# Optimization experiments

Measured on AMD Instinct MI355X. Metric: run time of the kernel, lower is better.

## Reference

```python
import jax, jax.numpy as jnp
import numpy as np

NUM_CAPSULE = 16
DIM_CAPSULE = 32
ROUTINGS = 4
EPS = 1e-07


def squash(x, axis=-1):
    # NOTE: faithful to the source: x / sqrt(sum(x^2) + eps) (unit-norm style),
    # NOT the standard Hinton squash.
    s2 = jnp.sum(x * x, axis=axis, keepdims=True)
    return x / jnp.sqrt(s2 + EPS)


def setup_inputs() -> dict:
    key = jax.random.key(0)
    k1, k2 = jax.random.split(key)
    B, N_in, D_in = 128, 1024, 256
    x = jax.random.normal(k1, (B, N_in, D_in), dtype=jnp.float32)
    # xavier_normal over (1, D_in, NUM_CAPSULE*DIM_CAPSULE)
    fan_in, fan_out = D_in, NUM_CAPSULE * DIM_CAPSULE
    std = np.sqrt(2.0 / (fan_in + fan_out))
    W = jax.random.normal(k2, (1, D_in, NUM_CAPSULE * DIM_CAPSULE), dtype=jnp.float32) * std
    return {"x": x, "W": W}


def reference(x, W):
    B, N_in, _ = x.shape
    # u_hat: [B, N_in, num_cap*dim_cap] -> [B, num_cap, N_in, dim_cap]
    u_hat = jnp.matmul(x, W[0])
    u_hat = u_hat.reshape(B, N_in, NUM_CAPSULE, DIM_CAPSULE).transpose(0, 2, 1, 3)

    b = jnp.zeros((B, NUM_CAPSULE, N_in), dtype=u_hat.dtype)
    outputs = None
    for i in range(ROUTINGS):
        # torch permutes to softmax over the num_capsule axis; equivalent to axis=1 here
        c = jax.nn.softmax(b, axis=1)                      # [B, num_cap, N_in]
        outputs = squash(jnp.einsum('bij,bijk->bik', c, u_hat))  # [B, num_cap, dim_cap]
        if i < ROUTINGS - 1:
            b = jnp.einsum('bik,bijk->bij', outputs, u_hat)
    return outputs
```

## Files before the change

### kernel.cpp

```cpp
#include <hip/hip_runtime.h>
#include <hip/hip_bf16.h>

typedef unsigned int u32;
typedef float f32x4 __attribute__((ext_vector_type(4)));
typedef __bf16 bf16x8 __attribute__((ext_vector_type(8)));

#define BATCH 128
#define NIN   1024
#define DIN   256
#define NC    16
#define DC    32
#define NCOL  512

__device__ __forceinline__ float bflo(u32 v){ return __uint_as_float(v << 16); }
__device__ __forceinline__ float bfhi(u32 v){ return __uint_as_float(v & 0xffff0000u); }
__device__ __forceinline__ u32 bfround(u32 ua){ return (ua + 0x7fffu + ((ua >> 16) & 1u)) >> 16; }
__device__ __forceinline__ u32 pack2(float a, float b){
    return (bfround(__float_as_uint(a)) & 0xffffu) | (bfround(__float_as_uint(b)) << 16);
}
__device__ __forceinline__ bf16x8 ldfrag(const u32* p){
    return __builtin_bit_cast(bf16x8, *(const uint4*)p);
}

__global__ __launch_bounds__(256) void k_wconv(const float* __restrict__ W, uint4* __restrict__ Wt2){
    int id = blockIdx.x * 256 + threadIdx.x;
    int l = id & 63, ks = (id >> 6) & 7, ntile = id >> 9;
    int n = ntile * 16 + (l & 15);
    int w0 = ks * 16 + (l >> 4) * 4;
    u32 r[4];
    #pragma unroll
    for (int e = 0; e < 4; e++){
        int w = w0 + e;
        r[e] = pack2(W[(size_t)(2 * w) * NCOL + n], W[(size_t)(2 * w + 1) * NCOL + n]);
    }
    Wt2[id] = make_uint4(r[0], r[1], r[2], r[3]);
}

__global__ __launch_bounds__(512) void k_gemm(const float* __restrict__ x, const uint4* __restrict__ Wt2,
                                              u32* __restrict__ uhat, float* __restrict__ y0){
    __shared__ __align__(16) u32 xl[64 * 128];
    const int t = threadIdx.x, jb = blockIdx.x, b = blockIdx.y;
    const int lane = t & 63, wv = t >> 6;
    const int l15 = lane & 15, q = lane >> 4;

    {
        const float4* xg = (const float4*)(x + ((size_t)b * NIN + jb * 64) * DIN);
        #pragma unroll
        for (int m = 0; m < 4; m++){
            int p = t + 512 * m;
            float4 a = xg[2 * p], c = xg[2 * p + 1];
            int j = p >> 5, wq = 4 * (p & 31);
            uint4 v;
            v.x = pack2(a.x, a.y); v.y = pack2(a.z, a.w);
            v.z = pack2(c.x, c.y); v.w = pack2(c.z, c.w);
            *(uint4*)&xl[j * 128 + ((wq + 4 * j) & 127)] = v;
        }
    }
    __syncthreads();

    f32x4 acc[4][4];
    #pragma unroll
    for (int mt = 0; mt < 4; mt++)
        #pragma unroll
        for (int nt = 0; nt < 4; nt++) acc[mt][nt] = (f32x4){0.f, 0.f, 0.f, 0.f};
    #pragma unroll
    for (int ks = 0; ks < 8; ks++){
        bf16x8 af[4], bfr[4];
        #pragma unroll
        for (int mt = 0; mt < 4; mt++){
            int jr = mt * 16 + l15;
            af[mt] = ldfrag(&xl[jr * 128 + ((ks * 16 + q * 4 + 4 * jr) & 127)]);
        }
        #pragma unroll
        for (int nt = 0; nt < 4; nt++)
            bfr[nt] = __builtin_bit_cast(bf16x8, Wt2[(size_t)(((wv * 4 + nt) * 8 + ks) * 64) + lane]);
        #pragma unroll
        for (int mt = 0; mt < 4; mt++)
            #pragma unroll
            for (int nt = 0; nt < 4; nt++)
                acc[mt][nt] = __builtin_amdgcn_mfma_f32_16x16x32_bf16(af[mt], bfr[nt], acc[mt][nt], 0, 0, 0);
    }

    #pragma unroll
    for (int nt = 0; nt < 4; nt++){
        float v = 0.f;
        #pragma unroll
        for (int mt = 0; mt < 4; mt++)
            #pragma unroll
            for (int r = 0; r < 4; r++) v += acc[mt][nt][r];
        v += __shfl_xor(v, 16);
        v += __shfl_xor(v, 32);
        if (lane < 16) atomicAdd(&y0[b * NCOL + wv * 64 + nt * 16 + lane], v);
    }

    u32* ub = uhat + (((size_t)b * NC + jb) * NCOL) * 32;
    #pragma unroll
    for (int nt = 0; nt < 4; nt++){
        int n = wv * 64 + nt * 16 + l15;
        #pragma unroll
        for (int mt = 0; mt < 4; mt++){
            uint2 v;
            v.x = pack2(acc[mt][nt][0], acc[mt][nt][1]);
            v.y = pack2(acc[mt][nt][2], acc[mt][nt][3]);
            *(uint2*)&ub[n * 32 + mt * 8 + q * 2] = v;
        }
    }
}

__device__ __forceinline__ int rot8(int n){ return (n + (n >> 3)) & 7; }

__global__ __launch_bounds__(256) void k_route_u(const u32* __restrict__ uhat, const float* __restrict__ o,
                                                 float* __restrict__ y){
    __shared__ __align__(16) u32 ul[NCOL * 32];
    __shared__ float ol[NCOL];
    __shared__ float bbc[NC * 68];
    const int jc = blockIdx.x, b = blockIdx.y, t = threadIdx.x;

    ol[t] = o[b * NCOL + t];
    ol[t + 256] = o[b * NCOL + t + 256];
    {
        const uint4* ug = (const uint4*)(uhat + ((size_t)(b * NC + jc)) * NCOL * 32);
        #pragma unroll
        for (int m = 0; m < 16; m++){
            int id = t + 256 * m;
            int n = id >> 3, jq = id & 7;
            ((uint4*)ul)[n * 8 + ((jq + rot8(n)) & 7)] = ug[id];
        }
    }
    __syncthreads();

    {
        int i = t >> 4, jq2 = t & 15;
        float o_[32];
        #pragma unroll
        for (int e = 0; e < 8; e++) *(float4*)&o_[4 * e] = *(const float4*)&ol[i * DC + 4 * e];
        float a0 = 0.f, a1 = 0.f, a2 = 0.f, a3 = 0.f;
        #pragma unroll
        for (int k = 0; k < 32; k++){
            int n = i * DC + k;
            uint2 v = *(const uint2*)&ul[n * 32 + ((2 * jq2 + 4 * rot8(n)) & 31)];
            float ok = o_[k];
            a0 += ok * bflo(v.x); a1 += ok * bfhi(v.x);
            a2 += ok * bflo(v.y); a3 += ok * bfhi(v.y);
        }
        *(float4*)&bbc[i * 68 + 4 * jq2] = make_float4(a0, a1, a2, a3);
    }
    __syncthreads();

    if (t < 64){
        float m = -1e30f;
        #pragma unroll
        for (int i = 0; i < NC; i++) m = fmaxf(m, bbc[i * 68 + t]);
        float s = 0.f;
        #pragma unroll
        for (int i = 0; i < NC; i++){ float e = __expf(bbc[i * 68 + t] - m); bbc[i * 68 + t] = e; s += e; }
        float inv = 1.f / s;
        #pragma unroll
        for (int i = 0; i < NC; i++) bbc[i * 68 + t] *= inv;
    }
    __syncthreads();

    #pragma unroll
    for (int h = 0; h < 2; h++){
        int n = t + 256 * h;
        int i = n >> 5;
        float s = 0.f;
        #pragma unroll
        for (int w4 = 0; w4 < 8; w4++){
            uint4 v = *(const uint4*)&ul[n * 32 + ((4 * w4 + 4 * rot8(n)) & 31)];
            float4 c0 = *(const float4*)&bbc[i * 68 + 8 * w4];
            float4 c1 = *(const float4*)&bbc[i * 68 + 8 * w4 + 4];
            s += c0.x * bflo(v.x) + c0.y * bfhi(v.x) + c0.z * bflo(v.y) + c0.w * bfhi(v.y)
               + c1.x * bflo(v.z) + c1.y * bfhi(v.z) + c1.z * bflo(v.w) + c1.w * bfhi(v.w);
        }
        atomicAdd(&y[b * NCOL + n], s);
    }
}

__global__ __launch_bounds__(512) void k_squash(const float* __restrict__ y, float* __restrict__ o,
                                                float* __restrict__ out, int final){
    int b = blockIdx.x, t = threadIdx.x;
    float v = y[b * NCOL + t];
    float s = v * v;
    s += __shfl_xor(s, 1); s += __shfl_xor(s, 2); s += __shfl_xor(s, 4);
    s += __shfl_xor(s, 8); s += __shfl_xor(s, 16);
    float r = v / sqrtf(s + 1e-7f);
    if (final) out[b * NCOL + t] = r;
    else       o[b * NCOL + t] = r;
}

extern "C" void kernel_launch(void* const* d_in, const int* in_sizes, int n_in,
                              void* d_out, int out_size, void* d_ws, size_t ws_size,
                              hipStream_t stream){
    const float* x = (const float*)d_in[0];
    const float* W = (const float*)d_in[1];
    float* out = (float*)d_out;
    float* f = (float*)d_ws;
    float* y    = f;
    float* o    = f + 65536;
    uint4* Wt2  = (uint4*)(f + 131072);
    u32*   uhat = (u32*)(f + 196608);

    hipMemsetAsync(y, 0, NCOL * BATCH * sizeof(float), stream);
    k_wconv<<<64, 256, 0, stream>>>(W, Wt2);
    k_gemm<<<dim3(16, BATCH), 512, 0, stream>>>(x, Wt2, uhat, y);
    k_squash<<<BATCH, 512, 0, stream>>>(y, o, out, 0);
    for (int it = 1; it < 4; it++){
        hipMemsetAsync(y, 0, NCOL * BATCH * sizeof(float), stream);
        k_route_u<<<dim3(16, BATCH), 256, 0, stream>>>(uhat, o, y);
        k_squash<<<BATCH, 512, 0, stream>>>(y, o, out, it == 3 ? 1 : 0);
    }
}
```

Baseline: 323.3 us.

## Reassociate routing through W to avoid materializing u_hat

The materialized u_hat tensor is dropped. Routing is re-expressed algebraically: the agreement logits become x·(W·o), and the weighted sum becomes (c^T x)·W, so each iteration works on x (bf16, transposed copy) and small per-batch vectors. A pre-kernel converts x to bf16 and also transposes it. It computes column sums for the first uniform-coupling iteration and converts W. The main kernel runs both contractions with MFMA and writes partial sums that a tail kernel reduces, multiplies by W, squashes, and projects back to v = W·o. This removes the large u_hat write and its repeated reads, at the cost of extra passes over x per iteration and new rounding points.

```diff
diff --git a/kernel.cpp b/kernel.cpp
--- a/kernel.cpp
+++ b/kernel.cpp
@@ -1,7 +1,7 @@
 #include <hip/hip_runtime.h>
-#include <hip/hip_bf16.h>
 
 typedef unsigned int u32;
+typedef unsigned short u16;
 typedef float f32x4 __attribute__((ext_vector_type(4)));
 typedef __bf16 bf16x8 __attribute__((ext_vector_type(8)));
 
@@ -18,175 +18,179 @@
 __device__ __forceinline__ u32 pack2(float a, float b){
     return (bfround(__float_as_uint(a)) & 0xffffu) | (bfround(__float_as_uint(b)) << 16);
 }
-__device__ __forceinline__ bf16x8 ldfrag(const u32* p){
-    return __builtin_bit_cast(bf16x8, *(const uint4*)p);
-}
-
-__global__ __launch_bounds__(256) void k_wconv(const float* __restrict__ W, uint4* __restrict__ Wt2){
-    int id = blockIdx.x * 256 + threadIdx.x;
-    int l = id & 63, ks = (id >> 6) & 7, ntile = id >> 9;
-    int n = ntile * 16 + (l & 15);
-    int w0 = ks * 16 + (l >> 4) * 4;
-    u32 r[4];
-    #pragma unroll
-    for (int e = 0; e < 4; e++){
-        int w = w0 + e;
-        r[e] = pack2(W[(size_t)(2 * w) * NCOL + n], W[(size_t)(2 * w + 1) * NCOL + n]);
-    }
-    Wt2[id] = make_uint4(r[0], r[1], r[2], r[3]);
-}
-
-__global__ __launch_bounds__(512) void k_gemm(const float* __restrict__ x, const uint4* __restrict__ Wt2,
-                                              u32* __restrict__ uhat, float* __restrict__ y0){
-    __shared__ __align__(16) u32 xl[64 * 128];
-    const int t = threadIdx.x, jb = blockIdx.x, b = blockIdx.y;
+
+__device__ __forceinline__ int lds_x(int r, int d){
+    int sw = (d >> 2) ^ ((r & 7) << 1) ^ (((r >> 3) & 3) << 2);
+    return r * 256 + (sw << 2) + (d & 3);
+}
+
+__global__ __launch_bounds__(256) void k_pre(const float* __restrict__ x, const float* __restrict__ W,
+                                             uint4* __restrict__ xbT, float* __restrict__ s,
+                                             uint2* __restrict__ Wb){
+    __shared__ __align__(16) u16 xt[64 * 256];
+    const int t = threadIdx.x, jc8 = blockIdx.x, b = blockIdx.y;
+
+    if (jc8 == 0){
+        float4 w4 = ((const float4*)W)[b * 256 + t];
+        Wb[b * 256 + t] = make_uint2(pack2(w4.x, w4.y), pack2(w4.z, w4.w));
+    }
+    {
+        const float4* xg = (const float4*)(x + ((size_t)b * NIN + jc8 * 64) * DIN);
+        int d4 = t & 63;
+        #pragma unroll
+        for (int m = 0; m < 16; m++){
+            int r = (t >> 6) + 4 * m;
+            float4 v = xg[r * 64 + d4];
+            *(uint2*)&xt[lds_x(r, d4 * 4)] = make_uint2(pack2(v.x, v.y), pack2(v.z, v.w));
+        }
+    }
+    __syncthreads();
+    {
+        float acc = 0.f;
+        #pragma unroll
+        for (int r = 0; r < 64; r++) acc += bflo((u32)xt[lds_x(r, t)]);
+        atomicAdd(&s[b * DIN + t], acc);
+    }
+    #pragma unroll
+    for (int w = 0; w < 8; w++){
+        int oid = t + 256 * w;
+        int lane = oid & 63, js2 = (oid >> 6) & 1, dt = oid >> 7;
+        int l15 = lane & 15, q = lane >> 4;
+        int rb = js2 * 32 + q * 8, d = dt * 16 + l15;
+        u32 r[4];
+        #pragma unroll
+        for (int p = 0; p < 4; p++){
+            u32 lo = xt[lds_x(rb + 2 * p, d)];
+            u32 hi = xt[lds_x(rb + 2 * p + 1, d)];
+            r[p] = lo | (hi << 16);
+        }
+        xbT[(((size_t)b * 16 + dt) * 32 + (jc8 * 2 + js2)) * 64 + lane] = make_uint4(r[0], r[1], r[2], r[3]);
+    }
+}
+
+__global__ __launch_bounds__(256) void k_main(const float* __restrict__ x, const uint4* __restrict__ xbT,
+                                              const u16* __restrict__ vb, float* __restrict__ zp){
+    __shared__ float bbl[16][132];
+    __shared__ __align__(16) u16 cl[16][136];
+    const int t = threadIdx.x, jh = blockIdx.x, b = blockIdx.y;
     const int lane = t & 63, wv = t >> 6;
     const int l15 = lane & 15, q = lane >> 4;
 
+    uint4 vfrag[8];
+    #pragma unroll
+    for (int ks = 0; ks < 8; ks++)
+        vfrag[ks] = *(const uint4*)&vb[((size_t)b * 16 + l15) * 256 + ks * 32 + q * 8];
+
+    #pragma unroll
+    for (int u = 0; u < 2; u++){
+        int jt = wv * 2 + u;
+        const float* xr = x + ((size_t)b * NIN + jh * 128 + jt * 16 + l15) * DIN + q * 8;
+        float4 xa[8][2];
+        #pragma unroll
+        for (int ks = 0; ks < 8; ks++){
+            xa[ks][0] = *(const float4*)(xr + ks * 32);
+            xa[ks][1] = *(const float4*)(xr + ks * 32 + 4);
+        }
+        f32x4 acc = {0.f, 0.f, 0.f, 0.f};
+        #pragma unroll
+        for (int ks = 0; ks < 8; ks++){
+            uint4 xw;
+            xw.x = pack2(xa[ks][0].x, xa[ks][0].y);
+            xw.y = pack2(xa[ks][0].z, xa[ks][0].w);
+            xw.z = pack2(xa[ks][1].x, xa[ks][1].y);
+            xw.w = pack2(xa[ks][1].z, xa[ks][1].w);
+            acc = __builtin_amdgcn_mfma_f32_16x16x32_bf16(
+                __builtin_bit_cast(bf16x8, vfrag[ks]), __builtin_bit_cast(bf16x8, xw), acc, 0, 0, 0);
+        }
+        #pragma unroll
+        for (int r = 0; r < 4; r++) bbl[q * 4 + r][jt * 16 + l15] = acc[r];
+    }
+    __syncthreads();
+
+    if (t < 128){
+        float mx = -1e30f, e[16], sum = 0.f;
+        #pragma unroll
+        for (int i = 0; i < 16; i++) mx = fmaxf(mx, bbl[i][t]);
+        #pragma unroll
+        for (int i = 0; i < 16; i++){ e[i] = __expf(bbl[i][t] - mx); sum += e[i]; }
+        float inv = 1.f / sum;
+        #pragma unroll
+        for (int i = 0; i < 16; i++) cl[i][t] = (u16)bfround(__float_as_uint(e[i] * inv));
+    }
+    __syncthreads();
+
+    bf16x8 cfrag[4];
+    #pragma unroll
+    for (int ksj = 0; ksj < 4; ksj++)
+        cfrag[ksj] = __builtin_bit_cast(bf16x8, *(const uint4*)&cl[l15][ksj * 32 + q * 8]);
+    #pragma unroll
+    for (int u = 0; u < 4; u++){
+        int dt = wv * 4 + u;
+        f32x4 acc = {0.f, 0.f, 0.f, 0.f};
+        #pragma unroll
+        for (int ksj = 0; ksj < 4; ksj++){
+            uint4 bw = xbT[(((size_t)b * 16 + dt) * 32 + jh * 4 + ksj) * 64 + lane];
+            acc = __builtin_amdgcn_mfma_f32_16x16x32_bf16(
+                cfrag[ksj], __builtin_bit_cast(bf16x8, bw), acc, 0, 0, 0);
+        }
+        float* zpb = zp + ((((size_t)jh * 128 + b) * 16) * 256) + dt * 16 + l15;
+        #pragma unroll
+        for (int r = 0; r < 4; r++) zpb[(size_t)(q * 4 + r) * 256] = acc[r];
+    }
+}
+
+__global__ __launch_bounds__(512) void k_tail(const float* __restrict__ s, const float* __restrict__ zp,
+                                              const u16* __restrict__ Wb, u16* __restrict__ vb,
+                                              float* __restrict__ out, int mode){
+    __shared__ float zl[16][260];
+    __shared__ __align__(16) float ol[512];
+    const int b = blockIdx.x, t = threadIdx.x;
+    const int i = t >> 5;
+    float y = 0.f;
+    if (mode == 0){
+        if (t < 256) zl[0][t] = s[b * 256 + t] * (1.f / 16.f);
+        __syncthreads();
+        #pragma unroll 8
+        for (int d = 0; d < 256; d++) y += zl[0][d] * bflo((u32)Wb[d * 512 + t]);
+    } else {
+        #pragma unroll
+        for (int u0 = 0; u0 < 8; u0++){
+            int idx = t + 512 * u0;
+            int ii = idx >> 8, dd = idx & 255;
+            float acc = 0.f;
+            #pragma unroll
+            for (int jh = 0; jh < 8; jh++)
+                acc += zp[((((size_t)jh * 128 + b) * 16 + ii) * 256) + dd];
+            zl[ii][dd] = acc;
+        }
+        __syncthreads();
+        #pragma unroll 8
+        for (int d = 0; d < 256; d++) y += zl[i][d] * bflo((u32)Wb[d * 512 + t]);
+    }
+    float s2 = y * y;
+    s2 += __shfl_xor(s2, 1); s2 += __shfl_xor(s2, 2); s2 += __shfl_xor(s2, 4);
+    s2 += __shfl_xor(s2, 8); s2 += __shfl_xor(s2, 16);
+    float r = y / sqrtf(s2 + 1e-7f);
+    if (mode == 2){ out[b * 512 + t] = r; return; }
+    ol[t] = r;
+    __syncthreads();
     {
-        const float4* xg = (const float4*)(x + ((size_t)b * NIN + jb * 64) * DIN);
-        #pragma unroll
-        for (int m = 0; m < 4; m++){
-            int p = t + 512 * m;
-            float4 a = xg[2 * p], c = xg[2 * p + 1];
-            int j = p >> 5, wq = 4 * (p & 31);
-            uint4 v;
-            v.x = pack2(a.x, a.y); v.y = pack2(a.z, a.w);
-            v.z = pack2(c.x, c.y); v.w = pack2(c.z, c.w);
-            *(uint4*)&xl[j * 128 + ((wq + 4 * j) & 127)] = v;
-        }
-    }
-    __syncthreads();
-
-    f32x4 acc[4][4];
-    #pragma unroll
-    for (int mt = 0; mt < 4; mt++)
-        #pragma unroll
-        for (int nt = 0; nt < 4; nt++) acc[mt][nt] = (f32x4){0.f, 0.f, 0.f, 0.f};
-    #pragma unroll
-    for (int ks = 0; ks < 8; ks++){
-        bf16x8 af[4], bfr[4];
-        #pragma unroll
-        for (int mt = 0; mt < 4; mt++){
-            int jr = mt * 16 + l15;
-            af[mt] = ldfrag(&xl[jr * 128 + ((ks * 16 + q * 4 + 4 * jr) & 127)]);
-        }
-        #pragma unroll
-        for (int nt = 0; nt < 4; nt++)
-            bfr[nt] = __builtin_bit_cast(bf16x8, Wt2[(size_t)(((wv * 4 + nt) * 8 + ks) * 64) + lane]);
-        #pragma unroll
-        for (int mt = 0; mt < 4; mt++)
+        int d = t & 255, ih = t >> 8;
+        #pragma unroll
+        for (int ii2 = 0; ii2 < 8; ii2++){
+            int i2 = ih * 8 + ii2;
+            const float4* op = (const float4*)&ol[i2 * 32];
+            float acc = 0.f;
             #pragma unroll
-            for (int nt = 0; nt < 4; nt++)
-                acc[mt][nt] = __builtin_amdgcn_mfma_f32_16x16x32_bf16(af[mt], bfr[nt], acc[mt][nt], 0, 0, 0);
-    }
-
-    #pragma unroll
-    for (int nt = 0; nt < 4; nt++){
-        float v = 0.f;
-        #pragma unroll
-        for (int mt = 0; mt < 4; mt++)
-            #pragma unroll
-            for (int r = 0; r < 4; r++) v += acc[mt][nt][r];
-        v += __shfl_xor(v, 16);
-        v += __shfl_xor(v, 32);
-        if (lane < 16) atomicAdd(&y0[b * NCOL + wv * 64 + nt * 16 + lane], v);
-    }
-
-    u32* ub = uhat + (((size_t)b * NC + jb) * NCOL) * 32;
-    #pragma unroll
-    for (int nt = 0; nt < 4; nt++){
-        int n = wv * 64 + nt * 16 + l15;
-        #pragma unroll
-        for (int mt = 0; mt < 4; mt++){
-            uint2 v;
-            v.x = pack2(acc[mt][nt][0], acc[mt][nt][1]);
-            v.y = pack2(acc[mt][nt][2], acc[mt][nt][3]);
-            *(uint2*)&ub[n * 32 + mt * 8 + q * 2] = v;
-        }
-    }
-}
-
-__device__ __forceinline__ int rot8(int n){ return (n + (n >> 3)) & 7; }
-
-__global__ __launch_bounds__(256) void k_route_u(const u32* __restrict__ uhat, const float* __restrict__ o,
-                                                 float* __restrict__ y){
-    __shared__ __align__(16) u32 ul[NCOL * 32];
-    __shared__ float ol[NCOL];
-    __shared__ float bbc[NC * 68];
-    const int jc = blockIdx.x, b = blockIdx.y, t = threadIdx.x;
-
-    ol[t] = o[b * NCOL + t];
-    ol[t + 256] = o[b * NCOL + t + 256];
-    {
-        const uint4* ug = (const uint4*)(uhat + ((size_t)(b * NC + jc)) * NCOL * 32);
-        #pragma unroll
-        for (int m = 0; m < 16; m++){
-            int id = t + 256 * m;
-            int n = id >> 3, jq = id & 7;
-            ((uint4*)ul)[n * 8 + ((jq + rot8(n)) & 7)] = ug[id];
-        }
-    }
-    __syncthreads();
-
-    {
-        int i = t >> 4, jq2 = t & 15;
-        float o_[32];
-        #pragma unroll
-        for (int e = 0; e < 8; e++) *(float4*)&o_[4 * e] = *(const float4*)&ol[i * DC + 4 * e];
-        float a0 = 0.f, a1 = 0.f, a2 = 0.f, a3 = 0.f;
-        #pragma unroll
-        for (int k = 0; k < 32; k++){
-            int n = i * DC + k;
-            uint2 v = *(const uint2*)&ul[n * 32 + ((2 * jq2 + 4 * rot8(n)) & 31)];
-            float ok = o_[k];
-            a0 += ok * bflo(v.x); a1 += ok * bfhi(v.x);
-            a2 += ok * bflo(v.y); a3 += ok * bfhi(v.y);
-        }
-        *(float4*)&bbc[i * 68 + 4 * jq2] = make_float4(a0, a1, a2, a3);
-    }
-    __syncthreads();
-
-    if (t < 64){
-        float m = -1e30f;
-        #pragma unroll
-        for (int i = 0; i < NC; i++) m = fmaxf(m, bbc[i * 68 + t]);
-        float s = 0.f;
-        #pragma unroll
-        for (int i = 0; i < NC; i++){ float e = __expf(bbc[i * 68 + t] - m); bbc[i * 68 + t] = e; s += e; }
-        float inv = 1.f / s;
-        #pragma unroll
-        for (int i = 0; i < NC; i++) bbc[i * 68 + t] *= inv;
-    }
-    __syncthreads();
-
-    #pragma unroll
-    for (int h = 0; h < 2; h++){
-        int n = t + 256 * h;
-        int i = n >> 5;
-        float s = 0.f;
-        #pragma unroll
-        for (int w4 = 0; w4 < 8; w4++){
-            uint4 v = *(const uint4*)&ul[n * 32 + ((4 * w4 + 4 * rot8(n)) & 31)];
-            float4 c0 = *(const float4*)&bbc[i * 68 + 8 * w4];
-            float4 c1 = *(const float4*)&bbc[i * 68 + 8 * w4 + 4];
-            s += c0.x * bflo(v.x) + c0.y * bfhi(v.x) + c0.z * bflo(v.y) + c0.w * bfhi(v.y)
-               + c1.x * bflo(v.z) + c1.y * bfhi(v.z) + c1.z * bflo(v.w) + c1.w * bfhi(v.w);
-        }
-        atomicAdd(&y[b * NCOL + n], s);
-    }
-}
-
-__global__ __launch_bounds__(512) void k_squash(const float* __restrict__ y, float* __restrict__ o,
-                                                float* __restrict__ out, int final){
-    int b = blockIdx.x, t = threadIdx.x;
-    float v = y[b * NCOL + t];
-    float s = v * v;
-    s += __shfl_xor(s, 1); s += __shfl_xor(s, 2); s += __shfl_xor(s, 4);
-    s += __shfl_xor(s, 8); s += __shfl_xor(s, 16);
-    float r = v / sqrtf(s + 1e-7f);
-    if (final) out[b * NCOL + t] = r;
-    else       o[b * NCOL + t] = r;
+            for (int w4 = 0; w4 < 4; w4++){
+                uint4 wv4 = *(const uint4*)&Wb[(size_t)d * 512 + i2 * 32 + w4 * 8];
+                float4 o0 = op[w4 * 2], o1 = op[w4 * 2 + 1];
+                acc += o0.x * bflo(wv4.x) + o0.y * bfhi(wv4.x) + o0.z * bflo(wv4.y) + o0.w * bfhi(wv4.y)
+                     + o1.x * bflo(wv4.z) + o1.y * bfhi(wv4.z) + o1.z * bflo(wv4.w) + o1.w * bfhi(wv4.w);
+            }
+            vb[((size_t)b * 16 + i2) * 256 + d] = (u16)bfround(__float_as_uint(acc));
+        }
+    }
 }
 
 extern "C" void kernel_launch(void* const* d_in, const int* in_sizes, int n_in,
@@ -195,19 +199,18 @@
     const float* x = (const float*)d_in[0];
     const float* W = (const float*)d_in[1];
     float* out = (float*)d_out;
-    float* f = (float*)d_ws;
-    float* y    = f;
-    float* o    = f + 65536;
-    uint4* Wt2  = (uint4*)(f + 131072);
-    u32*   uhat = (u32*)(f + 196608);
-
-    hipMemsetAsync(y, 0, NCOL * BATCH * sizeof(float), stream);
-    k_wconv<<<64, 256, 0, stream>>>(W, Wt2);
-    k_gemm<<<dim3(16, BATCH), 512, 0, stream>>>(x, Wt2, uhat, y);
-    k_squash<<<BATCH, 512, 0, stream>>>(y, o, out, 0);
+    char* ws = (char*)d_ws;
+    float* s    = (float*)(ws);
+    u16*   vb   = (u16*)  (ws + 131072);
+    u16*   Wb   = (u16*)  (ws + 1179648);
+    float* zp   = (float*)(ws + 1441792);
+    uint4* xbT  = (uint4*)(ws + 18219008);
+
+    hipMemsetAsync(s, 0, 131072, stream);
+    k_pre<<<dim3(16, BATCH), 256, 0, stream>>>(x, W, xbT, s, (uint2*)Wb);
+    k_tail<<<BATCH, 512, 0, stream>>>(s, zp, Wb, vb, out, 0);
     for (int it = 1; it < 4; it++){
-        hipMemsetAsync(y, 0, NCOL * BATCH * sizeof(float), stream);
-        k_route_u<<<dim3(16, BATCH), 256, 0, stream>>>(uhat, o, y);
-        k_squash<<<BATCH, 512, 0, stream>>>(y, o, out, it == 3 ? 1 : 0);
-    }
-}
+        k_main<<<dim3(8, BATCH), 256, 0, stream>>>(x, xbT, vb, zp);
+        k_tail<<<BATCH, 512, 0, stream>>>(s, zp, Wb, vb, out, it == 3 ? 2 : 1);
+    }
+}
```

Result: slower. 371.8 us (+15.0%).
